# Optimization experiments

Hardware: AMD Instinct MI355X
Metric: run time of the kernel (lower is better)

## Reference

```python
import jax, jax.numpy as jnp
import numpy as np

SQRT2 = 1.4142135623730951  # fused_leaky_relu gain
DN = ('NCHW', 'OIHW', 'NCHW')


def _setup_filter():
    # upfirdn2d.setup_filter([1,3,3,1]): separable outer product, normalized to sum 1
    f = jnp.array([1., 3., 3., 1.], dtype=jnp.float32)
    f = f / jnp.sum(f)
    return jnp.outer(f, f)  # [4,4], symmetric so flip is a no-op


def _depthwise_fir(x, f2, pad, down):
    # upfirdn2d: depthwise conv with the 4x4 resample filter
    C = x.shape[1]
    k = jnp.broadcast_to(f2[None, None], (C, 1, 4, 4)).astype(x.dtype)
    return jax.lax.conv_general_dilated(
        x, k, window_strides=(down, down),
        padding=[(pad, pad), (pad, pad)],
        feature_group_count=C, dimension_numbers=DN)


def _conv(x, w, stride, pad):
    return jax.lax.conv_general_dilated(
        x, w, window_strides=(stride, stride),
        padding=[(pad, pad), (pad, pad)], dimension_numbers=DN)


def _act(x):
    # fused_leaky_relu with no bias: leaky_relu(x, 0.2) * sqrt(2)
    return jax.nn.leaky_relu(x, negative_slope=0.2) * SQRT2


def setup_inputs() -> dict:
    key = jax.random.key(0)
    k1, k2, k3, k4 = jax.random.split(key, 4)
    N, Cin, Cout, H = 16, 256, 512, 64
    return {
        'latents_in': jax.random.normal(k1, (N, Cin, H, H), dtype=jnp.float32),
        'w_conv': jax.random.normal(k2, (Cin, Cin, 3, 3), dtype=jnp.float32),
        'w_down': jax.random.normal(k3, (Cout, Cin, 3, 3), dtype=jnp.float32),
        'w_skip': jax.random.normal(k4, (Cout, Cin, 1, 1), dtype=jnp.float32),
    }


def reference(latents_in, w_conv, w_down, w_skip):
    f2 = _setup_filter()
    Cin = w_conv.shape[1]
    g3 = 1.0 / np.sqrt(Cin * 9)   # weight_gain for 3x3 convs
    g1 = 1.0 / np.sqrt(Cin)       # weight_gain for 1x1 skip conv

    y = latents_in
    # self.conv: 3x3, pad 1, stride 1, no bias, fused leaky relu
    x = _act(_conv(y, w_conv * g3, stride=1, pad=1))
    # self.conv_down: FIR lowpass (pad 2) then 3x3 conv stride 2 (conv2d_resample down=2)
    x = _depthwise_fir(x, f2, pad=2, down=1)          # [N,Cin,H+1,H+1]
    out = _act(_conv(x, w_down * g3, stride=2, pad=0))  # [N,Cout,H/2,H/2]
    # skip path: downsample2d(y) then 1x1 conv (no bias) + act
    skip = _depthwise_fir(y, f2, pad=1, down=2)       # [N,Cin,H/2,H/2]
    skip = _act(_conv(skip, w_skip * g1, stride=1, pad=0))
    return skip + out
```

## Files before the change

kernel.cpp:

```cpp
#include <hip/hip_runtime.h>
#include <hip/hip_bf16.h>
#include <stdint.h>


typedef __bf16 bf8v __attribute__((ext_vector_type(8)));
typedef float  f4   __attribute__((ext_vector_type(4)));

#define G3F (1.0f / 48.0f)
#define G1F (1.0f / 16.0f)
#define SQRT2F 1.4142135623730951f

__device__ __forceinline__ float actf(float v) {
    return (v > 0.0f ? v : 0.2f * v) * SQRT2F;
}
__device__ __forceinline__ unsigned short f2bu(float f) {
    __hip_bfloat16 h = __float2bfloat16(f);
    return *reinterpret_cast<unsigned short*>(&h);
}
__device__ __forceinline__ bf8v ld8(const __hip_bfloat16* p) {
    return *reinterpret_cast<const bf8v*>(p);
}
__device__ __forceinline__ void llds16(const __hip_bfloat16* g, void* l) {
    __builtin_amdgcn_global_load_lds(
        (const __attribute__((address_space(1))) unsigned int*)g,
        (__attribute__((address_space(3))) unsigned int*)l, 16, 0, 0);
}

__global__ __launch_bounds__(256) void p_pad(__hip_bfloat16* __restrict__ xb) {
    int idx = blockIdx.x * 256 + threadIdx.x;
    int c8 = idx & 31, side = (idx >> 5) & 1, h = (idx >> 6) & 63, n = idx >> 12;
    int wp = side * 65;
    uint4 z = {0, 0, 0, 0};
    *reinterpret_cast<uint4*>(xb + (((size_t)(n * 64 + h) * 66 + wp) << 8) + c8 * 8) = z;
}

__global__ __launch_bounds__(256) void p_xb(const float* __restrict__ lat,
                                            __hip_bfloat16* __restrict__ xb) {
    __shared__ float tile[32][65];
    int bx = blockIdx.x;
    int cic = bx & 7, h = (bx >> 3) & 63, n = bx >> 9;
    int ci0 = cic * 32;
    int t = threadIdx.x;
    {
        int cir = t >> 3, wq = (t & 7) * 8;
        const float* src = lat + (((size_t)(n * 256 + ci0 + cir) * 64 + h) * 64 + wq);
        float4 v0 = *(const float4*)src;
        float4 v1 = *(const float4*)(src + 4);
        tile[cir][wq + 0] = v0.x; tile[cir][wq + 1] = v0.y;
        tile[cir][wq + 2] = v0.z; tile[cir][wq + 3] = v0.w;
        tile[cir][wq + 4] = v1.x; tile[cir][wq + 5] = v1.y;
        tile[cir][wq + 6] = v1.z; tile[cir][wq + 7] = v1.w;
    }
    __syncthreads();
    {
        int w = t >> 2, c8 = (t & 3) * 8;
        union { uint4 q; unsigned short h8[8]; } pk;
        #pragma unroll
        for (int j = 0; j < 8; ++j) pk.h8[j] = f2bu(tile[c8 + j][w]);
        __hip_bfloat16* dst = xb + (((size_t)(n * 64 + h) * 66 + (w + 1)) << 8) + ci0 + c8;
        *reinterpret_cast<uint4*>(dst) = pk.q;
    }
}

__global__ __launch_bounds__(256) void p_wA(const float* __restrict__ w,
                                            __hip_bfloat16* __restrict__ wA) {
    int idx = blockIdx.x * 256 + threadIdx.x;
    int lane = idx & 63;
    int co16 = (idx >> 6) & 15;
    int q    = (idx >> 10) & 7;
    int t    = idx >> 13;
    int co = co16 * 16 + (lane & 15);
    int ci = q * 32 + (lane >> 4) * 8;
    union { uint4 v; unsigned short h8[8]; } pk;
    #pragma unroll
    for (int e = 0; e < 8; ++e)
        pk.h8[e] = f2bu(w[(size_t)(co * 256 + ci + e) * 9 + t] * G3F);
    *reinterpret_cast<uint4*>(wA + (size_t)idx * 8) = pk.v;
}
__global__ __launch_bounds__(256) void p_wD(const float* __restrict__ w,
                                            __hip_bfloat16* __restrict__ wD) {
    int idx = blockIdx.x * 256 + threadIdx.x;
    int lane = idx & 63;
    int co16 = (idx >> 6) & 31;
    int q    = (idx >> 11) & 7;
    int t    = idx >> 14;
    int co = co16 * 16 + (lane & 15);
    int ci = q * 32 + (lane >> 4) * 8;
    union { uint4 v; unsigned short h8[8]; } pk;
    #pragma unroll
    for (int e = 0; e < 8; ++e)
        pk.h8[e] = f2bu(w[(size_t)(co * 256 + ci + e) * 9 + t] * G3F);
    *reinterpret_cast<uint4*>(wD + (size_t)idx * 8) = pk.v;
}
__global__ __launch_bounds__(256) void p_ws(const float* __restrict__ w,
                                            __hip_bfloat16* __restrict__ wst) {
    int idx = blockIdx.x * 256 + threadIdx.x;
    wst[idx] = __float2bfloat16(w[idx] * G1F);
}

__global__ __launch_bounds__(256) void k_fir2n(const __hip_bfloat16* __restrict__ xb,
                                               __hip_bfloat16* __restrict__ s2) {
    int idx = blockIdx.x * 256 + threadIdx.x;
    int c8 = idx & 31, ow = (idx >> 5) & 31, oh = (idx >> 10) & 31, n = idx >> 15;
    const float fk[4] = {0.125f, 0.375f, 0.375f, 0.125f};
    float a8[8];
    #pragma unroll
    for (int e = 0; e < 8; ++e) a8[e] = 0.0f;
    const __hip_bfloat16* src = xb + ((size_t)n * 64 * 66) * 256 + c8 * 8;
    #pragma unroll
    for (int i = 0; i < 4; ++i) {
        int rr = 2 * oh + i - 1;
        if ((unsigned)rr >= 64u) continue;
        #pragma unroll
        for (int j = 0; j < 4; ++j) {
            int wp = 2 * ow + j;
            bf8v v = ld8(src + ((size_t)(rr * 66 + wp) << 8));
            float fw = fk[i] * fk[j];
            #pragma unroll
            for (int e = 0; e < 8; ++e) a8[e] += fw * (float)v[e];
        }
    }
    union { uint4 q; unsigned short h8[8]; } pk;
    #pragma unroll
    for (int e = 0; e < 8; ++e) pk.h8[e] = f2bu(a8[e]);
    *reinterpret_cast<uint4*>(s2 + (((size_t)(n * 1024 + oh * 32 + ow)) << 8) + c8 * 8) = pk.q;
}

__global__ __launch_bounds__(256) void k_skipg(const __hip_bfloat16* __restrict__ s2,
                                               const __hip_bfloat16* __restrict__ wst,
                                               float* __restrict__ out) {
    const int lane = threadIdx.x & 63;
    const int wid  = threadIdx.x >> 6;
    const int wr = wid & 1, wc = wid >> 1;
    const int l15 = lane & 15, g = lane >> 4;

    int raw = blockIdx.x;
    int lg  = (raw & 7) * 64 + (raw >> 3);
    int cot = lg >> 7, pxt = lg & 127;
    int n = pxt >> 3, oh0 = (pxt & 7) * 4;

    f4 acc[4][4];
    #pragma unroll
    for (int m = 0; m < 4; ++m)
        #pragma unroll
        for (int nf = 0; nf < 4; ++nf)
            #pragma unroll
            for (int e = 0; e < 4; ++e) acc[m][nf][e] = 0.0f;

    #pragma unroll
    for (int k = 0; k < 8; ++k) {
        bf8v a_[4], b_[4];
        #pragma unroll
        for (int nf = 0; nf < 4; ++nf) {
            int oh = oh0 + wc * 2 + (nf >> 1);
            int ow = (nf & 1) * 16 + l15;
            b_[nf] = ld8(s2 + (((size_t)(n * 1024 + oh * 32 + ow)) << 8) + k * 32 + g * 8);
        }
        #pragma unroll
        for (int m = 0; m < 4; ++m) {
            int co = cot * 128 + wr * 64 + m * 16 + l15;
            a_[m] = ld8(wst + (size_t)co * 256 + k * 32 + g * 8);
        }
        #pragma unroll
        for (int m = 0; m < 4; ++m)
            #pragma unroll
            for (int nf = 0; nf < 4; ++nf)
                acc[m][nf] = __builtin_amdgcn_mfma_f32_16x16x32_bf16(
                    a_[m], b_[nf], acc[m][nf], 0, 0, 0);
    }
    #pragma unroll
    for (int m = 0; m < 4; ++m)
        #pragma unroll
        for (int nf = 0; nf < 4; ++nf) {
            f4 v = acc[m][nf];
            int oh = oh0 + wc * 2 + (nf >> 1);
            int ow = (nf & 1) * 16 + l15;
            int co = cot * 128 + wr * 64 + m * 16 + 4 * g;
            #pragma unroll
            for (int r = 0; r < 4; ++r)
                out[((size_t)(n * 512 + co + r)) * 1024 + oh * 32 + ow] = actf(v[r]);
        }
}

__global__ __launch_bounds__(256, 4) void k_conv1s(const __hip_bfloat16* __restrict__ xb,
                                                   const __hip_bfloat16* __restrict__ wA,
                                                   __hip_bfloat16* __restrict__ x1) {
    __shared__ uint4 smq[2112];
    char* smc = (char*)smq;
    const int tid  = threadIdx.x;
    const int lane = tid & 63;
    const int wid  = tid >> 6;
    const int wr = wid & 1, wc = wid >> 1;
    const int l15 = lane & 15, g = lane >> 4;

    int raw = blockIdx.x;
    int lg  = (raw & 7) * 128 + (raw >> 3);
    int cot = lg >> 9, pxt = lg & 511;
    int n = pxt >> 5, h0 = (pxt & 31) * 2;
    const size_t nb66 = (size_t)n * 64 * 66 * 256;
    const size_t nb   = (size_t)n * 4096 * 256;
    const char* wAc = (const char*)wA;

    f4 acc[4][4];
    #pragma unroll
    for (int m = 0; m < 4; ++m)
        #pragma unroll
        for (int nf = 0; nf < 4; ++nf)
            #pragma unroll
            for (int e = 0; e < 4; ++e) acc[m][nf][e] = 0.0f;

    #pragma unroll 1
    for (int ch = 0; ch < 4; ++ch) {
        if (ch) __syncthreads();
        for (int li = wid; li < 33; li += 4) {
            int gi = li * 64 + lane;
            int row = (gi >= 1584) ? 3 : (gi >= 1056) ? 2 : (gi >= 528) ? 1 : 0;
            int rem = gi - row * 528;
            int wp = rem >> 3;
            int c8 = (rem & 7) ^ (wp & 7);
            int rc = h0 - 1 + row; rc = rc < 0 ? 0 : (rc > 63 ? 63 : rc);
            const __hip_bfloat16* src =
                xb + nb66 + (((size_t)(rc * 66 + wp)) << 8) + ch * 64 + c8 * 8;
            llds16(src, smc + li * 1024);
        }
        __syncthreads();

        #pragma unroll
        for (int kh = 0; kh < 3; ++kh) {
            int rrow = h0 + wc + kh - 1;
            bool rowok = (unsigned)rrow < 64u;
            #pragma unroll
            for (int kw = 0; kw < 3; ++kw) {
                #pragma unroll
                for (int qq = 0; qq < 2; ++qq) {
                    int c8r = qq * 4 + g;
                    bf8v b_[4];
                    #pragma unroll
                    for (int nf = 0; nf < 4; ++nf) {
                        int wp = nf * 16 + l15 + kw;
                        int off = (wc + kh) * 8448 + (wp * 8 + (c8r ^ (wp & 7))) * 16;
                        bf8v v = *(const bf8v*)(smc + off);
                        bf8v z = {};
                        b_[nf] = rowok ? v : z;
                    }
                    int q = ch * 2 + qq;
                    #pragma unroll
                    for (int m = 0; m < 4; ++m) {
                        bf8v a = *(const bf8v*)(wAc +
                            ((size_t)(((kh * 3 + kw) * 8 + q) * 16 + cot * 8 + wr * 4 + m) << 10) +
                            (lane << 4));
                        #pragma unroll
                        for (int nf = 0; nf < 4; ++nf)
                            acc[m][nf] = __builtin_amdgcn_mfma_f32_16x16x32_bf16(
                                a, b_[nf], acc[m][nf], 0, 0, 0);
                    }
                }
            }
        }
    }

    __syncthreads();
    #pragma unroll
    for (int m = 0; m < 4; ++m)
        #pragma unroll
        for (int nf = 0; nf < 4; ++nf) {
            int p = wc * 64 + nf * 16 + l15;
            int co4 = wr * 16 + m * 4 + g;
            int co4s = co4 ^ ((p & 15) << 1);
            union { unsigned long long u; unsigned short h4[4]; } pk;
            #pragma unroll
            for (int r = 0; r < 4; ++r) pk.h4[r] = f2bu(actf(acc[m][nf][r]));
            *reinterpret_cast<unsigned long long*>(smc + p * 256 + co4s * 8) = pk.u;
        }
    __syncthreads();
    {
        int p = tid >> 1, coh = tid & 1;
        int hh = h0 + (p >> 6), w = p & 63;
        __hip_bfloat16* dst = x1 + nb + (((size_t)(hh * 64 + w)) << 8) + cot * 128 + coh * 64;
        #pragma unroll
        for (int j = 0; j < 8; ++j) {
            int r2 = coh * 8 + j;
            int co4s = (2 * r2) ^ ((p & 15) << 1);
            uint4 v = *reinterpret_cast<const uint4*>(smc + p * 256 + co4s * 8);
            *reinterpret_cast<uint4*>(dst + j * 8) = v;
        }
    }
}

__global__ __launch_bounds__(256) void k_fir1(const __hip_bfloat16* __restrict__ x1,
                                              __hip_bfloat16* __restrict__ xf) {
    int idx = blockIdx.x * 256 + threadIdx.x;
    int c8 = idx & 31; int rest = idx >> 5;
    int ow = rest % 65; rest /= 65;
    int oh = rest % 65; int n = rest / 65;
    int ci = c8 * 8;
    const float fk[4] = {0.125f, 0.375f, 0.375f, 0.125f};
    float a8[8];
    #pragma unroll
    for (int e = 0; e < 8; ++e) a8[e] = 0.0f;
    #pragma unroll
    for (int i = 0; i < 4; ++i) {
        int r = oh + i - 2;
        if (r < 0 || r >= 64) continue;
        #pragma unroll
        for (int j = 0; j < 4; ++j) {
            int c = ow + j - 2;
            if (c < 0 || c >= 64) continue;
            bf8v v = ld8(x1 + ((size_t)(n * 4096) + r * 64 + c) * 256 + ci);
            float fw = fk[i] * fk[j];
            #pragma unroll
            for (int e = 0; e < 8; ++e) a8[e] += fw * (float)v[e];
        }
    }
    union { uint4 q; unsigned short h8[8]; } pk;
    #pragma unroll
    for (int e = 0; e < 8; ++e) pk.h8[e] = f2bu(a8[e]);
    *reinterpret_cast<uint4*>(xf + ((size_t)n * 4225 + oh * 65 + ow) * 256 + ci) = pk.q;
}

__global__ __launch_bounds__(256, 4) void k_downs(const __hip_bfloat16* __restrict__ xf,
                                                  const __hip_bfloat16* __restrict__ wD,
                                                  float* __restrict__ out) {
    __shared__ uint4 smq[1344];
    char* smc = (char*)smq;
    const int tid  = threadIdx.x;
    const int lane = tid & 63;
    const int wid  = tid >> 6;
    const int l15  = lane & 15, g = lane >> 4;

    int raw = blockIdx.x;
    int lg  = (raw & 7) * 128 + (raw >> 3);
    int cot = lg >> 8;
    int rest = lg & 255;
    int n = rest >> 4, oht = rest & 15;
    int r0 = oht * 4;
    const size_t nxf = (size_t)n * 4225 * 256;
    const char* wDc = (const char*)wD;

    f4 acc[2][4];
    #pragma unroll
    for (int m = 0; m < 2; ++m)
        #pragma unroll
        for (int nf = 0; nf < 4; ++nf)
            #pragma unroll
            for (int e = 0; e < 4; ++e) acc[m][nf][e] = 0.0f;

    #pragma unroll 1
    for (int ch = 0; ch < 8; ++ch) {
        if (ch) __syncthreads();
        for (int li = wid; li < 21; li += 4) {
            int gi = li * 64 + lane;
            if (gi > 1319) gi = 1319;
            int row = (gi >= 1056) ? 4 : (gi >= 792) ? 3 : (gi >= 528) ? 2 :
                      (gi >= 264) ? 1 : 0;
            int rem = gi - row * 264;
            int wpair = rem >> 3;
            int t4 = (rem & 7) ^ (wpair & 7);
            int odd = t4 >> 2, c8 = t4 & 3;
            int wp = wpair * 2 + odd; if (wp > 64) wp = 64;
            const __hip_bfloat16* src = xf + nxf +
                (((size_t)((r0 + row) * 65 + wp)) << 8) + ch * 32 + c8 * 8;
            llds16(src, smc + li * 1024);
        }
        __syncthreads();

        #pragma unroll
        for (int kh = 0; kh < 3; ++kh) {
            #pragma unroll
            for (int kw = 0; kw < 3; ++kw) {
                bf8v b_[4];
                #pragma unroll
                for (int nf = 0; nf < 4; ++nf) {
                    int ow = (nf & 1) * 16 + l15;
                    int wp = 2 * ow + kw;
                    int wpair = wp >> 1, odd = wp & 1;
                    int s8 = (g + 4 * odd) ^ (wpair & 7);
                    int off = ((2 * (nf >> 1) + kh) * 264 + wpair * 8 + s8) * 16;
                    b_[nf] = *(const bf8v*)(smc + off);
                }
                #pragma unroll
                for (int m = 0; m < 2; ++m) {
                    bf8v a = *(const bf8v*)(wDc +
                        ((size_t)(((kh * 3 + kw) * 8 + ch) * 32 + cot * 8 + wid * 2 + m) << 10) +
                        (lane << 4));
                    #pragma unroll
                    for (int nf = 0; nf < 4; ++nf)
                        acc[m][nf] = __builtin_amdgcn_mfma_f32_16x16x32_bf16(
                            a, b_[nf], acc[m][nf], 0, 0, 0);
                }
            }
        }
    }

    #pragma unroll
    for (int m = 0; m < 2; ++m)
        #pragma unroll
        for (int nf = 0; nf < 4; ++nf) {
            f4 v = acc[m][nf];
            int oh = oht * 2 + (nf >> 1);
            int ow = (nf & 1) * 16 + l15;
            int co = cot * 128 + wid * 32 + m * 16 + 4 * g;
            #pragma unroll
            for (int r = 0; r < 4; ++r) {
                size_t oi = ((size_t)(n * 512 + co + r)) * 1024 + oh * 32 + ow;
                out[oi] += actf(v[r]);
            }
        }
}

extern "C" void kernel_launch(void* const* d_in, const int* in_sizes, int n_in,
                              void* d_out, int out_size, void* d_ws, size_t ws_size,
                              hipStream_t stream) {
    const float* lat   = (const float*)d_in[0];
    const float* wconv = (const float*)d_in[1];
    const float* wdown = (const float*)d_in[2];
    const float* wskip = (const float*)d_in[3];
    float* out = (float*)d_out;

    char* base = (char*)d_ws;
    __hip_bfloat16* xb  = (__hip_bfloat16*)base;
    __hip_bfloat16* xf  = (__hip_bfloat16*)base;
    __hip_bfloat16* x1  = (__hip_bfloat16*)(base + 34611200);
    __hip_bfloat16* s2  = (__hip_bfloat16*)(base + 34611200);
    __hip_bfloat16* wA  = (__hip_bfloat16*)(base + 68165632);
    __hip_bfloat16* wD  = (__hip_bfloat16*)(base + 69345280);
    __hip_bfloat16* wst = (__hip_bfloat16*)(base + 71704576);

    hipLaunchKernelGGL(p_pad,   dim3(256),  dim3(256), 0, stream, xb);
    hipLaunchKernelGGL(p_xb,    dim3(8192), dim3(256), 0, stream, lat,   xb);
    hipLaunchKernelGGL(p_wA,    dim3(288),  dim3(256), 0, stream, wconv, wA);
    hipLaunchKernelGGL(p_wD,    dim3(576),  dim3(256), 0, stream, wdown, wD);
    hipLaunchKernelGGL(p_ws,    dim3(512),  dim3(256), 0, stream, wskip, wst);
    hipLaunchKernelGGL(k_fir2n, dim3(2048), dim3(256), 0, stream, xb, s2);
    hipLaunchKernelGGL(k_skipg, dim3(512),  dim3(256), 0, stream, s2, wst, out);
    hipLaunchKernelGGL(k_conv1s, dim3(1024), dim3(256), 0, stream, xb, wA, x1);
    hipLaunchKernelGGL(k_fir1,  dim3(8450), dim3(256), 0, stream, x1, xf);
    hipLaunchKernelGGL(k_downs, dim3(1024), dim3(256), 0, stream, xf, wD, out);
}
```

Before: 226.6 us.

## Separable FIR with column reuse, taller downsample-conv tiles, zero-row halo loads

The FIR lowpass kernel now computes four adjacent output columns per thread. It applies the filter separably, doing vertical sums per input column and then a horizontal combine, which cuts redundant global loads and multiplies. The stride-2 conv kernel doubles its output rows per block (8 accumulator fragments, larger LDS tile, half the blocks), so each weight fragment load is reused twice as much. The 3x3 conv now loads out-of-range halo rows from a small zero buffer instead of masking fragments after LDS reads. In exchange, the conv kernel uses more registers and LDS, which may lower occupancy. The FIR kernel also recomputes overlapping outputs at the clamped last column group.

```diff
diff --git a/kernel.cpp b/kernel.cpp
--- a/kernel.cpp
+++ b/kernel.cpp
@@ -26,12 +26,15 @@
         (__attribute__((address_space(3))) unsigned int*)l, 16, 0, 0);
 }
 
-__global__ __launch_bounds__(256) void p_pad(__hip_bfloat16* __restrict__ xb) {
+__global__ __launch_bounds__(256) void p_pad(__hip_bfloat16* __restrict__ xb,
+                                             __hip_bfloat16* __restrict__ zbuf) {
     int idx = blockIdx.x * 256 + threadIdx.x;
     int c8 = idx & 31, side = (idx >> 5) & 1, h = (idx >> 6) & 63, n = idx >> 12;
     int wp = side * 65;
     uint4 z = {0, 0, 0, 0};
     *reinterpret_cast<uint4*>(xb + (((size_t)(n * 64 + h) * 66 + wp) << 8) + c8 * 8) = z;
+    if (blockIdx.x == 0 && threadIdx.x < 64)
+        *reinterpret_cast<uint4*>(zbuf + (threadIdx.x << 3)) = z;
 }
 
 __global__ __launch_bounds__(256) void p_xb(const float* __restrict__ lat,
@@ -184,6 +187,7 @@
 
 __global__ __launch_bounds__(256, 4) void k_conv1s(const __hip_bfloat16* __restrict__ xb,
                                                    const __hip_bfloat16* __restrict__ wA,
+                                                   const __hip_bfloat16* __restrict__ zbuf,
                                                    __hip_bfloat16* __restrict__ x1) {
     __shared__ uint4 smq[2112];
     char* smc = (char*)smq;
@@ -218,17 +222,16 @@
             int rem = gi - row * 528;
             int wp = rem >> 3;
             int c8 = (rem & 7) ^ (wp & 7);
-            int rc = h0 - 1 + row; rc = rc < 0 ? 0 : (rc > 63 ? 63 : rc);
-            const __hip_bfloat16* src =
-                xb + nb66 + (((size_t)(rc * 66 + wp)) << 8) + ch * 64 + c8 * 8;
+            int rc = h0 - 1 + row;
+            const __hip_bfloat16* src = ((unsigned)rc < 64u)
+                ? xb + nb66 + (((size_t)(rc * 66 + wp)) << 8) + ch * 64 + c8 * 8
+                : zbuf + (lane << 3);
             llds16(src, smc + li * 1024);
         }
         __syncthreads();
 
         #pragma unroll
         for (int kh = 0; kh < 3; ++kh) {
-            int rrow = h0 + wc + kh - 1;
-            bool rowok = (unsigned)rrow < 64u;
             #pragma unroll
             for (int kw = 0; kw < 3; ++kw) {
                 #pragma unroll
@@ -239,9 +242,7 @@
                     for (int nf = 0; nf < 4; ++nf) {
                         int wp = nf * 16 + l15 + kw;
                         int off = (wc + kh) * 8448 + (wp * 8 + (c8r ^ (wp & 7))) * 16;
-                        bf8v v = *(const bf8v*)(smc + off);
-                        bf8v z = {};
-                        b_[nf] = rowok ? v : z;
+                        b_[nf] = *(const bf8v*)(smc + off);
                     }
                     int q = ch * 2 + qq;
                     #pragma unroll
@@ -291,37 +292,48 @@
                                               __hip_bfloat16* __restrict__ xf) {
     int idx = blockIdx.x * 256 + threadIdx.x;
     int c8 = idx & 31; int rest = idx >> 5;
-    int ow = rest % 65; rest /= 65;
+    int owq = rest % 17; rest /= 17;
     int oh = rest % 65; int n = rest / 65;
+    int ow0 = owq * 4; if (ow0 > 61) ow0 = 61;
     int ci = c8 * 8;
     const float fk[4] = {0.125f, 0.375f, 0.375f, 0.125f};
-    float a8[8];
-    #pragma unroll
-    for (int e = 0; e < 8; ++e) a8[e] = 0.0f;
-    #pragma unroll
-    for (int i = 0; i < 4; ++i) {
-        int r = oh + i - 2;
-        if (r < 0 || r >= 64) continue;
-        #pragma unroll
-        for (int j = 0; j < 4; ++j) {
-            int c = ow + j - 2;
-            if (c < 0 || c >= 64) continue;
-            bf8v v = ld8(x1 + ((size_t)(n * 4096) + r * 64 + c) * 256 + ci);
-            float fw = fk[i] * fk[j];
-            #pragma unroll
-            for (int e = 0; e < 8; ++e) a8[e] += fw * (float)v[e];
-        }
-    }
-    union { uint4 q; unsigned short h8[8]; } pk;
-    #pragma unroll
-    for (int e = 0; e < 8; ++e) pk.h8[e] = f2bu(a8[e]);
-    *reinterpret_cast<uint4*>(xf + ((size_t)n * 4225 + oh * 65 + ow) * 256 + ci) = pk.q;
+    const __hip_bfloat16* src = x1 + (size_t)n * 4096 * 256 + ci;
+
+    float t[7][8];
+    #pragma unroll
+    for (int c = 0; c < 7; ++c) {
+        #pragma unroll
+        for (int e = 0; e < 8; ++e) t[c][e] = 0.0f;
+        int col = ow0 - 2 + c;
+        if ((unsigned)col >= 64u) continue;
+        #pragma unroll
+        for (int i = 0; i < 4; ++i) {
+            int r = oh + i - 2;
+            if ((unsigned)r >= 64u) continue;
+            bf8v v = ld8(src + ((size_t)(r * 64 + col) << 8));
+            float fw = fk[i];
+            #pragma unroll
+            for (int e = 0; e < 8; ++e) t[c][e] += fw * (float)v[e];
+        }
+    }
+    #pragma unroll
+    for (int o = 0; o < 4; ++o) {
+        union { uint4 q; unsigned short h8[8]; } pk;
+        #pragma unroll
+        for (int e = 0; e < 8; ++e) {
+            float s = fk[0] * t[o][e] + fk[1] * t[o + 1][e] +
+                      fk[2] * t[o + 2][e] + fk[3] * t[o + 3][e];
+            pk.h8[e] = f2bu(s);
+        }
+        *reinterpret_cast<uint4*>(
+            xf + ((size_t)n * 4225 + oh * 65 + ow0 + o) * 256 + ci) = pk.q;
+    }
 }
 
 __global__ __launch_bounds__(256, 4) void k_downs(const __hip_bfloat16* __restrict__ xf,
                                                   const __hip_bfloat16* __restrict__ wD,
                                                   float* __restrict__ out) {
-    __shared__ uint4 smq[1344];
+    __shared__ uint4 smq[2432];
     char* smc = (char*)smq;
     const int tid  = threadIdx.x;
     const int lane = tid & 63;
@@ -329,30 +341,29 @@
     const int l15  = lane & 15, g = lane >> 4;
 
     int raw = blockIdx.x;
-    int lg  = (raw & 7) * 128 + (raw >> 3);
-    int cot = lg >> 8;
-    int rest = lg & 255;
-    int n = rest >> 4, oht = rest & 15;
-    int r0 = oht * 4;
+    int lg  = (raw & 7) * 64 + (raw >> 3);
+    int cot = lg >> 7;
+    int rest = lg & 127;
+    int n = rest >> 3, oht = rest & 7;
+    int r0 = oht * 8;
     const size_t nxf = (size_t)n * 4225 * 256;
     const char* wDc = (const char*)wD;
 
-    f4 acc[2][4];
+    f4 acc[2][8];
     #pragma unroll
     for (int m = 0; m < 2; ++m)
         #pragma unroll
-        for (int nf = 0; nf < 4; ++nf)
+        for (int nf = 0; nf < 8; ++nf)
             #pragma unroll
             for (int e = 0; e < 4; ++e) acc[m][nf][e] = 0.0f;
 
     #pragma unroll 1
     for (int ch = 0; ch < 8; ++ch) {
         if (ch) __syncthreads();
-        for (int li = wid; li < 21; li += 4) {
+        for (int li = wid; li < 38; li += 4) {
             int gi = li * 64 + lane;
-            if (gi > 1319) gi = 1319;
-            int row = (gi >= 1056) ? 4 : (gi >= 792) ? 3 : (gi >= 528) ? 2 :
-                      (gi >= 264) ? 1 : 0;
+            if (gi > 2375) gi = 2375;
+            int row = gi / 264;
             int rem = gi - row * 264;
             int wpair = rem >> 3;
             int t4 = (rem & 7) ^ (wpair & 7);
@@ -368,9 +379,9 @@
         for (int kh = 0; kh < 3; ++kh) {
             #pragma unroll
             for (int kw = 0; kw < 3; ++kw) {
-                bf8v b_[4];
+                bf8v b_[8];
                 #pragma unroll
-                for (int nf = 0; nf < 4; ++nf) {
+                for (int nf = 0; nf < 8; ++nf) {
                     int ow = (nf & 1) * 16 + l15;
                     int wp = 2 * ow + kw;
                     int wpair = wp >> 1, odd = wp & 1;
@@ -384,7 +395,7 @@
                         ((size_t)(((kh * 3 + kw) * 8 + ch) * 32 + cot * 8 + wid * 2 + m) << 10) +
                         (lane << 4));
                     #pragma unroll
-                    for (int nf = 0; nf < 4; ++nf)
+                    for (int nf = 0; nf < 8; ++nf)
                         acc[m][nf] = __builtin_amdgcn_mfma_f32_16x16x32_bf16(
                             a, b_[nf], acc[m][nf], 0, 0, 0);
                 }
@@ -395,9 +406,9 @@
     #pragma unroll
     for (int m = 0; m < 2; ++m)
         #pragma unroll
-        for (int nf = 0; nf < 4; ++nf) {
+        for (int nf = 0; nf < 8; ++nf) {
             f4 v = acc[m][nf];
-            int oh = oht * 2 + (nf >> 1);
+            int oh = oht * 4 + (nf >> 1);
             int ow = (nf & 1) * 16 + l15;
             int co = cot * 128 + wid * 32 + m * 16 + 4 * g;
             #pragma unroll
@@ -418,22 +429,23 @@
     float* out = (float*)d_out;
 
     char* base = (char*)d_ws;
-    __hip_bfloat16* xb  = (__hip_bfloat16*)base;
-    __hip_bfloat16* xf  = (__hip_bfloat16*)base;
-    __hip_bfloat16* x1  = (__hip_bfloat16*)(base + 34611200);
-    __hip_bfloat16* s2  = (__hip_bfloat16*)(base + 34611200);
-    __hip_bfloat16* wA  = (__hip_bfloat16*)(base + 68165632);
-    __hip_bfloat16* wD  = (__hip_bfloat16*)(base + 69345280);
-    __hip_bfloat16* wst = (__hip_bfloat16*)(base + 71704576);
-
-    hipLaunchKernelGGL(p_pad,   dim3(256),  dim3(256), 0, stream, xb);
+    __hip_bfloat16* xb   = (__hip_bfloat16*)base;
+    __hip_bfloat16* xf   = (__hip_bfloat16*)base;
+    __hip_bfloat16* x1   = (__hip_bfloat16*)(base + 34611200);
+    __hip_bfloat16* s2   = (__hip_bfloat16*)(base + 34611200);
+    __hip_bfloat16* wA   = (__hip_bfloat16*)(base + 68165632);
+    __hip_bfloat16* wD   = (__hip_bfloat16*)(base + 69345280);
+    __hip_bfloat16* wst  = (__hip_bfloat16*)(base + 71704576);
+    __hip_bfloat16* zbuf = (__hip_bfloat16*)(base + 71966720);
+
+    hipLaunchKernelGGL(p_pad,   dim3(256),  dim3(256), 0, stream, xb, zbuf);
     hipLaunchKernelGGL(p_xb,    dim3(8192), dim3(256), 0, stream, lat,   xb);
     hipLaunchKernelGGL(p_wA,    dim3(288),  dim3(256), 0, stream, wconv, wA);
     hipLaunchKernelGGL(p_wD,    dim3(576),  dim3(256), 0, stream, wdown, wD);
     hipLaunchKernelGGL(p_ws,    dim3(512),  dim3(256), 0, stream, wskip, wst);
     hipLaunchKernelGGL(k_fir2n, dim3(2048), dim3(256), 0, stream, xb, s2);
     hipLaunchKernelGGL(k_skipg, dim3(512),  dim3(256), 0, stream, s2, wst, out);
-    hipLaunchKernelGGL(k_conv1s, dim3(1024), dim3(256), 0, stream, xb, wA, x1);
-    hipLaunchKernelGGL(k_fir1,  dim3(8450), dim3(256), 0, stream, x1, xf);
-    hipLaunchKernelGGL(k_downs, dim3(1024), dim3(256), 0, stream, xf, wD, out);
-}
+    hipLaunchKernelGGL(k_conv1s, dim3(1024), dim3(256), 0, stream, xb, wA, zbuf, x1);
+    hipLaunchKernelGGL(k_fir1,  dim3(2210), dim3(256), 0, stream, x1, xf);
+    hipLaunchKernelGGL(k_downs, dim3(512),  dim3(256), 0, stream, xf, wD, out);
+}
```

Result: slower. 396.6 us (+75.0%).
